# Kernel tuning notes

Measured on AMD Instinct MI355X. Metric: run time of the kernel, lower is better.

## Reference

```python
import jax, jax.numpy as jnp
import numpy as np

V_DIM, Q_DIM, NUM_HID = 2048, 1024, 1024
B, K, N = 64, 12, 36


def setup_inputs() -> dict:
    key = jax.random.key(0)
    ks = jax.random.split(key, 8)
    v = jax.random.normal(ks[0], (B, K, N, V_DIM), dtype=jnp.float32)
    q = jax.random.normal(ks[1], (B, K, Q_DIM), dtype=jnp.float32)
    # FCNet layer: weight_norm(Linear(v_dim+q_dim, num_hid), dim=None) + ReLU
    W1 = jax.random.normal(ks[2], (NUM_HID, V_DIM + Q_DIM), dtype=jnp.float32) * 0.02
    g1 = jnp.asarray(1.0, dtype=jnp.float32)  # weight_norm gain (scalar, dim=None)
    b1 = jnp.zeros((NUM_HID,), dtype=jnp.float32)
    # final: weight_norm(Linear(num_hid, 1), dim=None)
    W2 = jax.random.normal(ks[3], (1, NUM_HID), dtype=jnp.float32) * 0.02
    g2 = jnp.asarray(1.0, dtype=jnp.float32)
    b2 = jnp.zeros((1,), dtype=jnp.float32)
    return {"v": v, "q": q, "W1": W1, "g1": g1, "b1": b1, "W2": W2, "g2": g2, "b2": b2}


def reference(v, q, W1, g1, b1, W2, g2, b2):
    # weight_norm with dim=None: W_eff = g * W / ||W||_F (g is a scalar)
    W1e = g1 * W1 / jnp.linalg.norm(W1)   # [num_hid, v_dim+q_dim]
    W2e = g2 * W2 / jnp.linalg.norm(W2)   # [1, num_hid]
    # Avoid materializing the repeated+concatenated [B,K,N,v_dim+q_dim] tensor:
    # cat(v, broadcast(q)) @ W1e^T == v @ W1v^T + q @ W1q^T (q term broadcast over N)
    W1v = W1e[:, :V_DIM]                  # [num_hid, v_dim]
    W1q = W1e[:, V_DIM:]                  # [num_hid, q_dim]
    hv = jnp.einsum('bknv,hv->bknh', v, W1v)          # [B,K,N,num_hid]
    hq = jnp.einsum('bkq,hq->bkh', q, W1q)            # [B,K,num_hid]
    joint = jax.nn.relu(hv + hq[:, :, None, :] + b1)  # FCNet: weight-norm Linear + ReLU
    logits = jnp.einsum('bknh,oh->bkno', joint, W2e) + b2  # [B,K,N,1]
    w = jax.nn.softmax(logits, axis=1)                # softmax over k (dim 1)
    return w
```

## Files before the change

### kernel.cpp

```cpp
#include <hip/hip_runtime.h>

#define V_DIM   2048
#define Q_DIM   1024
#define NUM_HID 1024
#define BB 64
#define KK 12
#define NN 36
#define M_ROWS (BB*KK*NN)
#define BKROWS (BB*KK)

typedef unsigned short u16;
typedef __bf16 bf16x8  __attribute__((ext_vector_type(8)));
typedef u16    ushort8 __attribute__((ext_vector_type(8)));
typedef float  floatx4 __attribute__((ext_vector_type(4)));

__device__ __forceinline__ u16 f2bf(float f) {
    unsigned u = __float_as_uint(f);
    u += 0x7fffu + ((u >> 16) & 1u);
    return (u16)(u >> 16);
}

__global__ void norm_w1_kernel(const float* __restrict__ W1, float* __restrict__ acc)
{
    float s = 0.f;
    const float4* p = (const float4*)W1;
    const int total = (NUM_HID * (V_DIM + Q_DIM)) / 4;
    for (int i = blockIdx.x * 256 + threadIdx.x; i < total; i += 256 * 256) {
        float4 f = p[i];
        s += f.x * f.x + f.y * f.y + f.z * f.z + f.w * f.w;
    }
    #pragma unroll
    for (int off = 32; off > 0; off >>= 1) s += __shfl_down(s, off);
    __shared__ float red[4];
    if ((threadIdx.x & 63) == 0) red[threadIdx.x >> 6] = s;
    __syncthreads();
    if (threadIdx.x == 0) atomicAdd(acc, red[0] + red[1] + red[2] + red[3]);
}

__global__ void scale_kernel(const float* __restrict__ W2, const float* __restrict__ g1,
                             const float* __restrict__ g2, float* __restrict__ wsf)
{
    float v = W2[threadIdx.x];
    float s = v * v;
    #pragma unroll
    for (int off = 32; off > 0; off >>= 1) s += __shfl_down(s, off);
    __shared__ float red[16];
    if ((threadIdx.x & 63) == 0) red[threadIdx.x >> 6] = s;
    __syncthreads();
    if (threadIdx.x == 0) {
        float t = 0.f;
        #pragma unroll
        for (int u = 0; u < 16; u++) t += red[u];
        wsf[2] = g1[0] / sqrtf(wsf[0]);
        wsf[3] = g2[0] / sqrtf(t);
    }
}

__global__ void convert_w1_kernel(const float* __restrict__ W1,
                                  u16* __restrict__ W1v, u16* __restrict__ W1q)
{
    int s = blockIdx.x * 256 + threadIdx.x;
    if (s >= NUM_HID * (V_DIM + Q_DIM) / 8) return;
    int h = s / 384, g = s % 384;
    const float4* p = (const float4*)(W1 + (size_t)h * (V_DIM + Q_DIM) + g * 8);
    float4 a = p[0], b = p[1];
    ushort8 o;
    o[0]=f2bf(a.x); o[1]=f2bf(a.y); o[2]=f2bf(a.z); o[3]=f2bf(a.w);
    o[4]=f2bf(b.x); o[5]=f2bf(b.y); o[6]=f2bf(b.z); o[7]=f2bf(b.w);
    if (g < 256) *(ushort8*)(W1v + (size_t)h * V_DIM + g * 8) = o;
    else         *(ushort8*)(W1q + (size_t)h * Q_DIM + (g - 256) * 8) = o;
}

template<int GK, bool MAIN>
__global__ __launch_bounds__(256, 2)
void gemm_kernel(const float* __restrict__ Asrc,
                 const u16*   __restrict__ Bsrc,
                 float*       __restrict__ outp,
                 const float* __restrict__ hq,
                 const float* __restrict__ b1,
                 const float* __restrict__ W2,
                 const float* __restrict__ scl)
{
    __shared__ u16 As[128 * 72];
    __shared__ u16 Bs[128 * 72];

    const int tid  = threadIdx.x;
    const int lane = tid & 63;
    const int wv   = tid >> 6;
    const int wm   = wv & 1;
    const int wn   = wv >> 1;
    const int quad = lane >> 4;
    const int l15  = lane & 15;
    const int m0   = blockIdx.y * 128;
    const int n0   = blockIdx.x * 128;

    floatx4 acc[4][4];
    #pragma unroll
    for (int i = 0; i < 4; i++)
        #pragma unroll
        for (int j = 0; j < 4; j++)
            acc[i][j] = (floatx4){0.f, 0.f, 0.f, 0.f};

    for (int kt = 0; kt < GK / 64; ++kt) {
        const int k0 = kt * 64;
        __syncthreads();
        #pragma unroll
        for (int it = 0; it < 4; ++it) {
            int s = tid + 256 * it;
            int r = s >> 3, g = s & 7;
            const float4* gp = (const float4*)(Asrc + (size_t)(m0 + r) * GK + k0 + g * 8);
            float4 f0 = gp[0];
            float4 f1 = gp[1];
            ushort8 o;
            o[0]=f2bf(f0.x); o[1]=f2bf(f0.y); o[2]=f2bf(f0.z); o[3]=f2bf(f0.w);
            o[4]=f2bf(f1.x); o[5]=f2bf(f1.y); o[6]=f2bf(f1.z); o[7]=f2bf(f1.w);
            *(ushort8*)(&As[r * 72 + g * 8]) = o;
        }
        #pragma unroll
        for (int it = 0; it < 4; ++it) {
            int s = tid + 256 * it;
            int c = s >> 3, g = s & 7;
            ushort8 bv = *(const ushort8*)(Bsrc + (size_t)(n0 + c) * GK + k0 + g * 8);
            *(ushort8*)(&Bs[c * 72 + g * 8]) = bv;
        }
        __syncthreads();
        #pragma unroll
        for (int ks = 0; ks < 2; ++ks) {
            bf16x8 af[4], bfr[4];
            #pragma unroll
            for (int i = 0; i < 4; i++)
                af[i] = *(const bf16x8*)(&As[(wm * 64 + i * 16 + l15) * 72 + ks * 32 + quad * 8]);
            #pragma unroll
            for (int j = 0; j < 4; j++)
                bfr[j] = *(const bf16x8*)(&Bs[(wn * 64 + j * 16 + l15) * 72 + ks * 32 + quad * 8]);
            #pragma unroll
            for (int i = 0; i < 4; i++)
                #pragma unroll
                for (int j = 0; j < 4; j++)
                    acc[i][j] = __builtin_amdgcn_mfma_f32_16x16x32_bf16(af[i], bfr[j], acc[i][j], 0, 0, 0);
        }
    }

    if constexpr (MAIN) {
        const float s1 = scl[2];
        int   cg[4];
        float w2v[4], b1v[4];
        #pragma unroll
        for (int j = 0; j < 4; j++) {
            cg[j]  = n0 + wn * 64 + j * 16 + l15;
            w2v[j] = W2[cg[j]];
            b1v[j] = b1[cg[j]];
        }
        #pragma unroll
        for (int i = 0; i < 4; i++) {
            #pragma unroll
            for (int r = 0; r < 4; r++) {
                const int mg = m0 + wm * 64 + i * 16 + quad * 4 + r;
                const int bk = mg / NN;
                float p = 0.f;
                #pragma unroll
                for (int j = 0; j < 4; j++) {
                    float pre = s1 * (acc[i][j][r] + hq[(size_t)bk * NUM_HID + cg[j]]) + b1v[j];
                    p += fmaxf(pre, 0.f) * w2v[j];
                }
                p += __shfl_xor(p, 1);
                p += __shfl_xor(p, 2);
                p += __shfl_xor(p, 4);
                p += __shfl_xor(p, 8);
                if (l15 == 0)
                    outp[(size_t)mg * 16 + blockIdx.x * 2 + wn] = p;
            }
        }
    } else {
        #pragma unroll
        for (int i = 0; i < 4; i++)
            #pragma unroll
            for (int r = 0; r < 4; r++) {
                const int mg = m0 + wm * 64 + i * 16 + quad * 4 + r;
                #pragma unroll
                for (int j = 0; j < 4; j++) {
                    const int c = n0 + wn * 64 + j * 16 + l15;
                    outp[(size_t)mg * NUM_HID + c] = acc[i][j][r];
                }
            }
    }
}

__global__ void softmax_kernel(const float* __restrict__ part,
                               const float* __restrict__ scl,
                               const float* __restrict__ b2,
                               float* __restrict__ out)
{
    int t = blockIdx.x * 256 + threadIdx.x;
    if (t >= BB * NN) return;
    int b = t / NN, n = t % NN;
    float s2 = scl[3], bias = b2[0];
    float lg[KK];
    float mx = -1e30f;
    #pragma unroll
    for (int k = 0; k < KK; k++) {
        int m = (b * KK + k) * NN + n;
        const float4* pp = (const float4*)(part + (size_t)m * 16);
        float4 a0 = pp[0], a1 = pp[1], a2 = pp[2], a3 = pp[3];
        float s = (a0.x + a0.y + a0.z + a0.w) + (a1.x + a1.y + a1.z + a1.w)
                + (a2.x + a2.y + a2.z + a2.w) + (a3.x + a3.y + a3.z + a3.w);
        lg[k] = s2 * s + bias;
        mx = fmaxf(mx, lg[k]);
    }
    float den = 0.f;
    #pragma unroll
    for (int k = 0; k < KK; k++) { lg[k] = expf(lg[k] - mx); den += lg[k]; }
    float inv = 1.0f / den;
    #pragma unroll
    for (int k = 0; k < KK; k++) out[(size_t)((b * KK + k) * NN + n)] = lg[k] * inv;
}

extern "C" void kernel_launch(void* const* d_in, const int* in_sizes, int n_in,
                              void* d_out, int out_size, void* d_ws, size_t ws_size,
                              hipStream_t stream)
{
    (void)in_sizes; (void)n_in; (void)out_size; (void)ws_size;
    const float* v  = (const float*)d_in[0];
    const float* q  = (const float*)d_in[1];
    const float* W1 = (const float*)d_in[2];
    const float* g1 = (const float*)d_in[3];
    const float* b1 = (const float*)d_in[4];
    const float* W2 = (const float*)d_in[5];
    const float* g2 = (const float*)d_in[6];
    const float* b2 = (const float*)d_in[7];
    float* out = (float*)d_out;

    char*  ws   = (char*)d_ws;
    float* wsf  = (float*)ws;
    float* hq   = (float*)(ws + 16);
    u16*   W1v  = (u16*)  (ws + 16 + 3145728);
    u16*   W1q  = (u16*)  (ws + 16 + 3145728 + 4194304);
    float* part = (float*)(ws + 16 + 3145728 + 4194304 + 2097152);

    hipMemsetAsync(d_ws, 0, 16, stream);
    norm_w1_kernel<<<256, 256, 0, stream>>>(W1, wsf);
    scale_kernel<<<1, 1024, 0, stream>>>(W2, g1, g2, wsf);
    convert_w1_kernel<<<1536, 256, 0, stream>>>(W1, W1v, W1q);
    gemm_kernel<Q_DIM, false><<<dim3(8, 6), 256, 0, stream>>>(q, W1q, hq, nullptr, nullptr, nullptr, wsf);
    gemm_kernel<V_DIM, true><<<dim3(8, 216), 256, 0, stream>>>(v, W1v, part, hq, b1, W2, wsf);
    softmax_kernel<<<9, 256, 0, stream>>>(part, wsf, b2, out);
}
```

Measured before the change: 592.2 us.

## Pre-convert v/q to bf16 and stream GEMM tiles via global_load_lds with XOR swizzle

Adds a separate pass that converts v and q to bf16 once, so the GEMM no longer reads fp32 and converts it in every N-tile block, which previously re-read v eight times. GEMM tiles are now loaded straight into LDS with global_load_lds, using an XOR-swizzled unpadded layout to avoid bank conflicts, and launch bounds are raised for occupancy. The W1 Frobenius norm is fused into the W1 convert kernel using wave-level atomics. The trade-off is an extra full write and read of a bf16 copy of v, about 113 MB.

```diff
diff --git a/kernel.cpp b/kernel.cpp
--- a/kernel.cpp
+++ b/kernel.cpp
@@ -14,53 +14,24 @@
 typedef u16    ushort8 __attribute__((ext_vector_type(8)));
 typedef float  floatx4 __attribute__((ext_vector_type(4)));
 
+#define AS1 __attribute__((address_space(1)))
+#define AS3 __attribute__((address_space(3)))
+
+__device__ __forceinline__ void gl_lds16(const void* g, void* l) {
+    __builtin_amdgcn_global_load_lds((const AS1 void*)g, (AS3 void*)l, 16, 0, 0);
+}
+
 __device__ __forceinline__ u16 f2bf(float f) {
     unsigned u = __float_as_uint(f);
     u += 0x7fffu + ((u >> 16) & 1u);
     return (u16)(u >> 16);
 }
 
-__global__ void norm_w1_kernel(const float* __restrict__ W1, float* __restrict__ acc)
-{
-    float s = 0.f;
-    const float4* p = (const float4*)W1;
-    const int total = (NUM_HID * (V_DIM + Q_DIM)) / 4;
-    for (int i = blockIdx.x * 256 + threadIdx.x; i < total; i += 256 * 256) {
-        float4 f = p[i];
-        s += f.x * f.x + f.y * f.y + f.z * f.z + f.w * f.w;
-    }
-    #pragma unroll
-    for (int off = 32; off > 0; off >>= 1) s += __shfl_down(s, off);
-    __shared__ float red[4];
-    if ((threadIdx.x & 63) == 0) red[threadIdx.x >> 6] = s;
-    __syncthreads();
-    if (threadIdx.x == 0) atomicAdd(acc, red[0] + red[1] + red[2] + red[3]);
-}
-
-__global__ void scale_kernel(const float* __restrict__ W2, const float* __restrict__ g1,
-                             const float* __restrict__ g2, float* __restrict__ wsf)
-{
-    float v = W2[threadIdx.x];
-    float s = v * v;
-    #pragma unroll
-    for (int off = 32; off > 0; off >>= 1) s += __shfl_down(s, off);
-    __shared__ float red[16];
-    if ((threadIdx.x & 63) == 0) red[threadIdx.x >> 6] = s;
-    __syncthreads();
-    if (threadIdx.x == 0) {
-        float t = 0.f;
-        #pragma unroll
-        for (int u = 0; u < 16; u++) t += red[u];
-        wsf[2] = g1[0] / sqrtf(wsf[0]);
-        wsf[3] = g2[0] / sqrtf(t);
-    }
-}
-
 __global__ void convert_w1_kernel(const float* __restrict__ W1,
-                                  u16* __restrict__ W1v, u16* __restrict__ W1q)
+                                  u16* __restrict__ W1v, u16* __restrict__ W1q,
+                                  float* __restrict__ acc)
 {
     int s = blockIdx.x * 256 + threadIdx.x;
-    if (s >= NUM_HID * (V_DIM + Q_DIM) / 8) return;
     int h = s / 384, g = s % 384;
     const float4* p = (const float4*)(W1 + (size_t)h * (V_DIM + Q_DIM) + g * 8);
     float4 a = p[0], b = p[1];
@@ -69,20 +40,62 @@
     o[4]=f2bf(b.x); o[5]=f2bf(b.y); o[6]=f2bf(b.z); o[7]=f2bf(b.w);
     if (g < 256) *(ushort8*)(W1v + (size_t)h * V_DIM + g * 8) = o;
     else         *(ushort8*)(W1q + (size_t)h * Q_DIM + (g - 256) * 8) = o;
+    float ss = a.x*a.x + a.y*a.y + a.z*a.z + a.w*a.w
+             + b.x*b.x + b.y*b.y + b.z*b.z + b.w*b.w;
+    #pragma unroll
+    for (int off = 32; off > 0; off >>= 1) ss += __shfl_down(ss, off);
+    if ((threadIdx.x & 63) == 0) atomicAdd(acc, ss);
+}
+
+#define VSLOTS (M_ROWS * V_DIM / 8)
+#define QSLOTS (BKROWS * Q_DIM / 8)
+__global__ void convert_vq_kernel(const float* __restrict__ v, const float* __restrict__ q,
+                                  u16* __restrict__ vbf, u16* __restrict__ qbf)
+{
+    int s = blockIdx.x * 256 + threadIdx.x;
+    const float* src;
+    u16* dst;
+    if (s < VSLOTS) { src = v; dst = vbf; }
+    else            { src = q; dst = qbf; s -= VSLOTS; }
+    const float4* p = (const float4*)src + (size_t)s * 2;
+    float4 a = p[0], b = p[1];
+    ushort8 o;
+    o[0]=f2bf(a.x); o[1]=f2bf(a.y); o[2]=f2bf(a.z); o[3]=f2bf(a.w);
+    o[4]=f2bf(b.x); o[5]=f2bf(b.y); o[6]=f2bf(b.z); o[7]=f2bf(b.w);
+    *(ushort8*)(dst + (size_t)s * 8) = o;
+}
+
+__global__ void scale_kernel(const float* __restrict__ W2, const float* __restrict__ g1,
+                             const float* __restrict__ g2, float* __restrict__ wsf)
+{
+    float v = W2[threadIdx.x];
+    float s = v * v;
+    #pragma unroll
+    for (int off = 32; off > 0; off >>= 1) s += __shfl_down(s, off);
+    __shared__ float red[16];
+    if ((threadIdx.x & 63) == 0) red[threadIdx.x >> 6] = s;
+    __syncthreads();
+    if (threadIdx.x == 0) {
+        float t = 0.f;
+        #pragma unroll
+        for (int u = 0; u < 16; u++) t += red[u];
+        wsf[2] = g1[0] / sqrtf(wsf[0]);
+        wsf[3] = g2[0] / sqrtf(t);
+    }
 }
 
 template<int GK, bool MAIN>
-__global__ __launch_bounds__(256, 2)
-void gemm_kernel(const float* __restrict__ Asrc,
-                 const u16*   __restrict__ Bsrc,
+__global__ __launch_bounds__(256, 3)
+void gemm_kernel(const u16* __restrict__ Abf,
+                 const u16* __restrict__ Bsrc,
                  float*       __restrict__ outp,
                  const float* __restrict__ hq,
                  const float* __restrict__ b1,
                  const float* __restrict__ W2,
                  const float* __restrict__ scl)
 {
-    __shared__ u16 As[128 * 72];
-    __shared__ u16 Bs[128 * 72];
+    __shared__ __align__(16) u16 As[128 * 64];
+    __shared__ __align__(16) u16 Bs[128 * 64];
 
     const int tid  = threadIdx.x;
     const int lane = tid & 63;
@@ -94,6 +107,14 @@
     const int m0   = blockIdx.y * 128;
     const int n0   = blockIdx.x * 128;
 
+    int rS[4], gS[4];
+    #pragma unroll
+    for (int j = 0; j < 4; j++) {
+        int p = (wv * 4 + j) * 64 + lane;
+        rS[j] = p >> 3;
+        gS[j] = (p & 7) ^ (rS[j] & 7);
+    }
+
     floatx4 acc[4][4];
     #pragma unroll
     for (int i = 0; i < 4; i++)
@@ -105,34 +126,26 @@
         const int k0 = kt * 64;
         __syncthreads();
         #pragma unroll
-        for (int it = 0; it < 4; ++it) {
-            int s = tid + 256 * it;
-            int r = s >> 3, g = s & 7;
-            const float4* gp = (const float4*)(Asrc + (size_t)(m0 + r) * GK + k0 + g * 8);
-            float4 f0 = gp[0];
-            float4 f1 = gp[1];
-            ushort8 o;
-            o[0]=f2bf(f0.x); o[1]=f2bf(f0.y); o[2]=f2bf(f0.z); o[3]=f2bf(f0.w);
-            o[4]=f2bf(f1.x); o[5]=f2bf(f1.y); o[6]=f2bf(f1.z); o[7]=f2bf(f1.w);
-            *(ushort8*)(&As[r * 72 + g * 8]) = o;
-        }
-        #pragma unroll
-        for (int it = 0; it < 4; ++it) {
-            int s = tid + 256 * it;
-            int c = s >> 3, g = s & 7;
-            ushort8 bv = *(const ushort8*)(Bsrc + (size_t)(n0 + c) * GK + k0 + g * 8);
-            *(ushort8*)(&Bs[c * 72 + g * 8]) = bv;
+        for (int j = 0; j < 4; j++) {
+            gl_lds16(Abf + (size_t)(m0 + rS[j]) * GK + k0 + gS[j] * 8,
+                     (char*)As + (wv * 4 + j) * 1024);
+            gl_lds16(Bsrc + (size_t)(n0 + rS[j]) * GK + k0 + gS[j] * 8,
+                     (char*)Bs + (wv * 4 + j) * 1024);
         }
         __syncthreads();
         #pragma unroll
         for (int ks = 0; ks < 2; ++ks) {
             bf16x8 af[4], bfr[4];
             #pragma unroll
-            for (int i = 0; i < 4; i++)
-                af[i] = *(const bf16x8*)(&As[(wm * 64 + i * 16 + l15) * 72 + ks * 32 + quad * 8]);
-            #pragma unroll
-            for (int j = 0; j < 4; j++)
-                bfr[j] = *(const bf16x8*)(&Bs[(wn * 64 + j * 16 + l15) * 72 + ks * 32 + quad * 8]);
+            for (int i = 0; i < 4; i++) {
+                int row = wm * 64 + i * 16 + l15;
+                af[i] = *(const bf16x8*)(&As[row * 64 + (((ks * 4 + quad) ^ (l15 & 7)) * 8)]);
+            }
+            #pragma unroll
+            for (int j = 0; j < 4; j++) {
+                int col = wn * 64 + j * 16 + l15;
+                bfr[j] = *(const bf16x8*)(&Bs[col * 64 + (((ks * 4 + quad) ^ (l15 & 7)) * 8)]);
+            }
             #pragma unroll
             for (int i = 0; i < 4; i++)
                 #pragma unroll
@@ -232,16 +245,18 @@
 
     char*  ws   = (char*)d_ws;
     float* wsf  = (float*)ws;
-    float* hq   = (float*)(ws + 16);
-    u16*   W1v  = (u16*)  (ws + 16 + 3145728);
-    u16*   W1q  = (u16*)  (ws + 16 + 3145728 + 4194304);
-    float* part = (float*)(ws + 16 + 3145728 + 4194304 + 2097152);
+    float* part = (float*)(ws + 16);
+    float* hqb  = (float*)(ws + 1769488);
+    u16*   W1v  = (u16*)  (ws + 4915216);
+    u16*   W1q  = (u16*)  (ws + 9109520);
+    u16*   qbf  = (u16*)  (ws + 11206672);
+    u16*   vbf  = (u16*)  (ws + 12779536);
 
     hipMemsetAsync(d_ws, 0, 16, stream);
-    norm_w1_kernel<<<256, 256, 0, stream>>>(W1, wsf);
+    convert_w1_kernel<<<1536, 256, 0, stream>>>(W1, W1v, W1q, wsf);
     scale_kernel<<<1, 1024, 0, stream>>>(W2, g1, g2, wsf);
-    convert_w1_kernel<<<1536, 256, 0, stream>>>(W1, W1v, W1q);
-    gemm_kernel<Q_DIM, false><<<dim3(8, 6), 256, 0, stream>>>(q, W1q, hq, nullptr, nullptr, nullptr, wsf);
-    gemm_kernel<V_DIM, true><<<dim3(8, 216), 256, 0, stream>>>(v, W1v, part, hq, b1, W2, wsf);
+    convert_vq_kernel<<<28032, 256, 0, stream>>>(v, q, vbf, qbf);
+    gemm_kernel<Q_DIM, false><<<dim3(8, 6), 256, 0, stream>>>(qbf, W1q, hqb, nullptr, nullptr, nullptr, wsf);
+    gemm_kernel<V_DIM, true><<<dim3(8, 216), 256, 0, stream>>>(vbf, W1v, part, hqb, b1, W2, wsf);
     softmax_kernel<<<9, 256, 0, stream>>>(part, wsf, b2, out);
 }
```

Result: slower. 634.4 us (+7.1%).
